# Kernel tuning notes

Hardware: AMD Instinct MI355X
Metric: run time of the kernel (lower is better)

## Reference

```python
import jax, jax.numpy as jnp
import numpy as np

EPS = 1e-7
N, L, BATCH = 512, 2, 128
N_IPF = 10


def setup_inputs() -> dict:
    key = jax.random.key(0)
    k1, k2, k3, k4 = jax.random.split(key, 4)
    return {
        "x": jax.random.randint(k1, (BATCH, N), 0, L, dtype=jnp.int32),
        "W": jax.random.normal(k2, (N, N), dtype=jnp.float32),
        "V_compress": jax.random.normal(k3, (N, L), dtype=jnp.float32),
        "E_compress": jax.random.normal(k4, (N, N, L, L), dtype=jnp.float32),
    }


def _moat_forward(W, V_compress, E_compress, x):
    n, l = V_compress.shape
    # marginals / joints
    V = jax.nn.softmax(V_compress, axis=1)              # (n, l)
    E = jnp.exp(E_compress)                              # (n, n, l, l)
    E = E / E.sum(axis=(-2, -1), keepdims=True)

    # 10-step Sinkhorn / IPF projection onto marginals V
    A_b = V[:, None, :, None]                            # (n, 1, l, 1)
    B_b = V[None, :, None, :]                            # (1, n, 1, l)
    for _ in range(N_IPF):
        row_marg = E.sum(axis=3, keepdims=True) + EPS    # (n, n, l, 1)
        col_marg = E.sum(axis=2, keepdims=True) + EPS    # (n, n, 1, l)
        E = E * (A_b / row_marg)
        E = E * (B_b / col_marg)
        E = E / (E.sum(axis=(-2, -1), keepdims=True) + EPS)

    # zero the diagonal (i == j) pairwise joints, clamp
    E = E * (1.0 - jnp.eye(n, dtype=E.dtype))[:, :, None, None]
    E = jnp.clip(E, 0.0, 1.0)

    # symmetric edge-weight matrix from strictly-lower-triangular sigmoid(W)
    Wm = jax.nn.sigmoid(W)
    Wm = jnp.tril(Wm, k=-1)
    Wm = Wm.T + Wm                                       # (n, n), zero diag
    L_0 = -Wm + jnp.diag(Wm.sum(axis=1))                 # graph Laplacian

    idx = jnp.arange(n)
    # Pr[b, i] = V[i, x[b, i]]
    Pr = V[idx[None, :], x]                              # (batch, n)
    # P[b, i, j] = E[i, j, x[b, i], x[b, j]]
    P = E[idx[None, :, None], idx[None, None, :], x[:, :, None], x[:, None, :]]  # (batch, n, n)
    P = P / (Pr[:, :, None] * Pr[:, None, :])

    WP = Wm[None, :, :] * P                              # (batch, n, n)
    Lb = -WP + jax.vmap(jnp.diag)(WP.sum(axis=2))        # batched Laplacian

    # matrix-tree theorem: logdet of the (n-1, n-1) principal minor
    _, logdet_L = jnp.linalg.slogdet(Lb[:, 1:, 1:])
    _, logdet_L0 = jnp.linalg.slogdet(L_0[1:, 1:])
    return jnp.log(Pr).sum(axis=1) + logdet_L - logdet_L0  # (batch,)


def reference(x, W, V_compress, E_compress):
    return _moat_forward(W, V_compress, E_compress, x)
```

## Files before the change

kernel.cpp:

```cpp
#include <hip/hip_runtime.h>
#include <hip/hip_bf16.h>
#include <math.h>

#define NDIM 512
#define NB   128
#define NMAT 129
#define EPSF 1e-7f
#define MS  ((size_t)262144)
#define LTS ((size_t)32768)
#define PSTR ((size_t)524288)

#define OFF_E   ((size_t)0)
#define OFF_WM  ((size_t)1048576)
#define OFF_IPR ((size_t)1310720)
#define OFF_LPR ((size_t)1376256)
#define OFF_LD  ((size_t)1376384)
#define OFF_MAT ((size_t)1377792)
#define OFF_LT  ((size_t)(OFF_MAT + (size_t)NMAT*MS))

__device__ __forceinline__ float rdlane(float v, int l) {
  return __uint_as_float((unsigned)__builtin_amdgcn_readlane((int)__float_as_uint(v), l));
}

__global__ __launch_bounds__(256) void k_prep(const float* __restrict__ W, const float* __restrict__ Vc,
                                              const float* __restrict__ Ec, float* __restrict__ Wm,
                                              float* __restrict__ E2) {
  int idx = blockIdx.x * 256 + threadIdx.x;
  int i = idx >> 9, j = idx & 511;
  float wv = 0.f;
  if (i > j)      wv = 1.f / (1.f + expf(-W[i*NDIM + j]));
  else if (i < j) wv = 1.f / (1.f + expf(-W[j*NDIM + i]));
  Wm[idx] = wv;
  float vi0 = Vc[2*i], vi1 = Vc[2*i+1];
  float mi = fmaxf(vi0, vi1);
  float ei0 = expf(vi0 - mi), ei1 = expf(vi1 - mi);
  float si = ei0 + ei1;
  float A0 = ei0 / si, A1 = ei1 / si;
  float vj0 = Vc[2*j], vj1 = Vc[2*j+1];
  float mj = fmaxf(vj0, vj1);
  float ej0 = expf(vj0 - mj), ej1 = expf(vj1 - mj);
  float sj = ej0 + ej1;
  float B0 = ej0 / sj, B1 = ej1 / sj;
  float4 ec = reinterpret_cast<const float4*>(Ec)[idx];
  float e00 = expf(ec.x), e01 = expf(ec.y), e10 = expf(ec.z), e11 = expf(ec.w);
  float s = e00 + e01 + e10 + e11;
  float inv = 1.f / s;
  e00 *= inv; e01 *= inv; e10 *= inv; e11 *= inv;
  for (int t = 0; t < 10; ++t) {
    float rm0 = e00 + e01 + EPSF, rm1 = e10 + e11 + EPSF;
    float cm0 = e00 + e10 + EPSF, cm1 = e01 + e11 + EPSF;
    float f0 = A0 / rm0, f1 = A1 / rm1;
    e00 *= f0; e01 *= f0; e10 *= f1; e11 *= f1;
    float g0 = B0 / cm0, g1 = B1 / cm1;
    e00 *= g0; e10 *= g0; e01 *= g1; e11 *= g1;
    float ss = e00 + e01 + e10 + e11 + EPSF;
    float iv = 1.f / ss;
    e00 *= iv; e01 *= iv; e10 *= iv; e11 *= iv;
  }
  if (i == j) { e00 = 0.f; e01 = 0.f; e10 = 0.f; e11 = 0.f; }
  e00 = fminf(fmaxf(e00, 0.f), 1.f);
  e01 = fminf(fmaxf(e01, 0.f), 1.f);
  e10 = fminf(fmaxf(e10, 0.f), 1.f);
  e11 = fminf(fmaxf(e11, 0.f), 1.f);
  reinterpret_cast<float2*>(E2)[idx]        = make_float2(e00, e01);
  reinterpret_cast<float2*>(E2 + PSTR)[idx] = make_float2(e10, e11);
}

__global__ __launch_bounds__(256) void k_Pr(const int* __restrict__ x, const float* __restrict__ Vc,
                                            float* __restrict__ invPr, float* __restrict__ logPr) {
  const int b = blockIdx.x;
  const int tid = threadIdx.x;
  float acc = 0.f;
  for (int ii = tid; ii < NDIM; ii += 256) {
    const int xv = x[b*NDIM + ii];
    float v0 = Vc[2*ii], v1 = Vc[2*ii+1];
    float mx = fmaxf(v0, v1);
    float e0 = expf(v0 - mx), e1 = expf(v1 - mx);
    float s = e0 + e1;
    const float p = xv ? (e1 / s) : (e0 / s);
    invPr[b*NDIM + ii] = 1.f / p;
    acc += logf(p);
  }
  for (int off = 32; off > 0; off >>= 1) acc += __shfl_down(acc, off, 64);
  __shared__ float sw[4];
  if ((tid & 63) == 0) sw[tid >> 6] = acc;
  __syncthreads();
  if (tid == 0) logPr[b] = sw[0] + sw[1] + sw[2] + sw[3];
}

__global__ __launch_bounds__(512) void k_build(const int* __restrict__ x, const float* __restrict__ E2,
                                               const float* __restrict__ Wm, const float* __restrict__ invPr,
                                               float* __restrict__ Mall) {
  const int b = blockIdx.x;
  const int i = blockIdx.y*8 + (threadIdx.x >> 6);
  const int lane = threadIdx.x & 63;
  const int j0 = lane << 3;

  const float4 w0 = *(const float4*)(Wm + (size_t)i*NDIM + j0);
  const float4 w1 = *(const float4*)(Wm + (size_t)i*NDIM + j0 + 4);
  float wp[8];
  if (b < NB) {
    const int   xi   = x[b*NDIM + i];
    const float ipri = invPr[b*NDIM + i];
    const int4  xa = *(const int4*)(x + b*NDIM + j0);
    const int4  xb = *(const int4*)(x + b*NDIM + j0 + 4);
    const float4 pa = *(const float4*)(invPr + b*NDIM + j0);
    const float4 pb = *(const float4*)(invPr + b*NDIM + j0 + 4);
    const float* pl = E2 + (size_t)xi*PSTR + ((size_t)i*NDIM + j0)*2;
    const float4 ea = *(const float4*)(pl);
    const float4 eb = *(const float4*)(pl + 4);
    const float4 ec = *(const float4*)(pl + 8);
    const float4 ed = *(const float4*)(pl + 12);
    wp[0] = w0.x * (xa.x ? ea.y : ea.x) * pa.x;
    wp[1] = w0.y * (xa.y ? ea.w : ea.z) * pa.y;
    wp[2] = w0.z * (xa.z ? eb.y : eb.x) * pa.z;
    wp[3] = w0.w * (xa.w ? eb.w : eb.z) * pa.w;
    wp[4] = w1.x * (xb.x ? ec.y : ec.x) * pb.x;
    wp[5] = w1.y * (xb.y ? ec.w : ec.z) * pb.y;
    wp[6] = w1.z * (xb.z ? ed.y : ed.x) * pb.z;
    wp[7] = w1.w * (xb.w ? ed.w : ed.z) * pb.w;
    #pragma unroll
    for (int k = 0; k < 8; ++k) wp[k] *= ipri;
  } else {
    wp[0]=w0.x; wp[1]=w0.y; wp[2]=w0.z; wp[3]=w0.w;
    wp[4]=w1.x; wp[5]=w1.y; wp[6]=w1.z; wp[7]=w1.w;
  }
  float s = ((wp[0]+wp[1])+(wp[2]+wp[3])) + ((wp[4]+wp[5])+(wp[6]+wp[7]));
  #pragma unroll
  for (int off = 32; off > 0; off >>= 1) s += __shfl_xor(s, off, 64);

  float o[8];
  #pragma unroll
  for (int k = 0; k < 8; ++k) o[k] = -wp[k];
  if (i == 0) {
    #pragma unroll
    for (int k = 0; k < 8; ++k) o[k] = 0.f;
    if (lane == 0) o[0] = 1.f;
  } else {
    if (lane == 0) o[0] = 0.f;
    #pragma unroll
    for (int k = 0; k < 8; ++k)
      if (j0 + k == i) o[k] = s;
  }
  float* dst = Mall + (size_t)b*MS + (size_t)i*NDIM + j0;
  *(float4*)(dst)   = make_float4(o[0],o[1],o[2],o[3]);
  *(float4*)(dst+4) = make_float4(o[4],o[5],o[6],o[7]);
}

template<int KK>
struct WFact {
  static __device__ __forceinline__ void run(float (&a)[64], const int lane,
                                             float& mypiv, float& myrec) {
    const float piv = rdlane(a[KK], KK);
    const float rec = 1.0f / piv;
    if (lane == KK) { mypiv = piv; myrec = rec; }
    if (lane > KK) {
      const float l = a[KK] * rec;
      a[KK] = l;
      #pragma unroll
      for (int c = KK + 1; c < 64; ++c)
        a[c] -= l * rdlane(a[c], KK);
    }
    WFact<KK + 1>::run(a, lane, mypiv, myrec);
  }
};
template<>
struct WFact<64> {
  static __device__ __forceinline__ void run(float (&)[64], int, float&, float&) {}
};

template<int C>
struct SolveStep {
  static __device__ __forceinline__ void run(float (&a)[64], const float (*T)[68]) {
    const float* Trow = T[C];
    float acc = a[C];
    #pragma unroll
    for (int p4 = 0; p4 + 4 <= C; p4 += 4) {
      const float4 tv = *(const float4*)(Trow + p4);
      acc -= a[p4+0] * tv.x;
      acc -= a[p4+1] * tv.y;
      acc -= a[p4+2] * tv.z;
      acc -= a[p4+3] * tv.w;
    }
    #pragma unroll
    for (int p = C & ~3; p < C; ++p) acc -= a[p] * Trow[p];
    a[C] = acc * Trow[66];
    SolveStep<C + 1>::run(a, T);
  }
};
template<>
struct SolveStep<64> {
  static __device__ __forceinline__ void run(float (&)[64], const float (*)[68]) {}
};

__global__ __launch_bounds__(128) void k_panel(float* __restrict__ Mall, float* __restrict__ Lt,
                                               float* __restrict__ logdets, int k0, int mrem) {
  const int b = blockIdx.x;
  const int sub = blockIdx.y;
  float* __restrict__ M = Mall + (size_t)b*MS;
  float* __restrict__ L = Lt + (size_t)b*LTS;
  const int t = threadIdx.x;
  __shared__ __align__(16) float T[64][68];

  if (t < 64) {
    float a[64];
    const float* row = M + (size_t)(k0+t)*NDIM + k0;
    #pragma unroll
    for (int c4 = 0; c4 < 16; ++c4) {
      float4 v = *(const float4*)(row + c4*4);
      a[c4*4+0]=v.x; a[c4*4+1]=v.y; a[c4*4+2]=v.z; a[c4*4+3]=v.w;
    }
    float mypiv = 1.f, myrec = 1.f;
    WFact<0>::run(a, t, mypiv, myrec);
    #pragma unroll
    for (int c = 0; c < 64; ++c) T[c][t] = a[c];
    T[t][66] = myrec;
    if (sub == 0) {
      float v = logf(fabsf(mypiv));
      #pragma unroll
      for (int off = 32; off > 0; off >>= 1) v += __shfl_down(v, off, 64);
      if (t == 0) logdets[b] = (k0 == 0) ? v : (logdets[b] + v);
    }
  }
  __syncthreads();

  if (mrem > 0) {
    if (t < 64) {
      const int col = k0 + 64 + sub*64 + t;
      float u[64];
      #pragma unroll
      for (int r = 0; r < 64; ++r) u[r] = M[(size_t)(k0+r)*NDIM + col];
      #pragma unroll
      for (int p = 0; p < 63; ++p) {
        const float lv = u[p];
        const float* Trow = T[p];
        const int kk0 = p + 1;
        const int kkA = (p + 4) & ~3;
        #pragma unroll
        for (int kk = kk0; kk < kkA; ++kk) u[kk] -= Trow[kk] * lv;
        #pragma unroll
        for (int kk4 = kkA; kk4 < 64; kk4 += 4) {
          const float4 tv = *(const float4*)(Trow + kk4);
          u[kk4+0] -= tv.x * lv;
          u[kk4+1] -= tv.y * lv;
          u[kk4+2] -= tv.z * lv;
          u[kk4+3] -= tv.w * lv;
        }
      }
      #pragma unroll
      for (int r = 1; r < 64; ++r) M[(size_t)(k0+r)*NDIM + col] = u[r];
    } else {
      const int lr = 64 + sub*64 + (t - 64);
      const int gr = k0 + lr;
      float a[64];
      const float* row = M + (size_t)gr*NDIM + k0;
      #pragma unroll
      for (int c4 = 0; c4 < 16; ++c4) {
        float4 v = *(const float4*)(row + c4*4);
        a[c4*4+0]=v.x; a[c4*4+1]=v.y; a[c4*4+2]=v.z; a[c4*4+3]=v.w;
      }
      SolveStep<0>::run(a, T);
      #pragma unroll
      for (int c = 0; c < 64; ++c) L[(size_t)c*NDIM + lr] = a[c];
    }
  }
}

__global__ __launch_bounds__(256, 4) void k_gemm(float* __restrict__ Mall, const float* __restrict__ Lt,
                                                 int k0) {
  const int b = blockIdx.x;
  float* __restrict__ M = Mall + (size_t)b*MS;
  const float* __restrict__ L = Lt + (size_t)b*LTS;
  __shared__ __align__(16) float As[64][68];
  __shared__ __align__(16) float Bs[64][68];
  const int tid = threadIdx.x;
  const int tx = tid & 15, ty = tid >> 4;
  const int rowbase = 64 + blockIdx.y*64;
  const int colbase = 64 + blockIdx.z*64;
  #pragma unroll
  for (int i = 0; i < 4; ++i) {
    int q = tid + 256*i;
    int p = q >> 4, f = q & 15;
    *(float4*)&As[p][f*4] = *(const float4*)&L[(size_t)p*NDIM + rowbase + f*4];
    *(float4*)&Bs[p][f*4] = *(const float4*)&M[(size_t)(k0+p)*NDIM + (k0+colbase) + f*4];
  }
  float* Crow = M + (size_t)(k0+rowbase+ty*4)*NDIM + (k0+colbase+tx*4);
  float4 c0 = *(float4*)(Crow + 0*NDIM);
  float4 c1 = *(float4*)(Crow + 1*NDIM);
  float4 c2 = *(float4*)(Crow + 2*NDIM);
  float4 c3 = *(float4*)(Crow + 3*NDIM);
  __syncthreads();
  #pragma unroll
  for (int p = 0; p < 64; ++p) {
    const float4 av = *(const float4*)&As[p][ty*4];
    const float4 bv = *(const float4*)&Bs[p][tx*4];
    c0.x -= av.x*bv.x; c0.y -= av.x*bv.y; c0.z -= av.x*bv.z; c0.w -= av.x*bv.w;
    c1.x -= av.y*bv.x; c1.y -= av.y*bv.y; c1.z -= av.y*bv.z; c1.w -= av.y*bv.w;
    c2.x -= av.z*bv.x; c2.y -= av.z*bv.y; c2.z -= av.z*bv.z; c2.w -= av.z*bv.w;
    c3.x -= av.w*bv.x; c3.y -= av.w*bv.y; c3.z -= av.w*bv.z; c3.w -= av.w*bv.w;
  }
  *(float4*)(Crow + 0*NDIM) = c0;
  *(float4*)(Crow + 1*NDIM) = c1;
  *(float4*)(Crow + 2*NDIM) = c2;
  *(float4*)(Crow + 3*NDIM) = c3;
}

__global__ void k_final(const float* __restrict__ logPr, const float* __restrict__ logdets,
                        float* __restrict__ out) {
  int t = threadIdx.x;
  if (t < NB) out[t] = logPr[t] + logdets[t] - logdets[NB];
}

extern "C" void kernel_launch(void* const* d_in, const int* in_sizes, int n_in,
                              void* d_out, int out_size, void* d_ws, size_t ws_size,
                              hipStream_t stream) {
  const int*   x  = (const int*)  d_in[0];
  const float* W  = (const float*)d_in[1];
  const float* Vc = (const float*)d_in[2];
  const float* Ec = (const float*)d_in[3];
  float* out = (float*)d_out;
  float* ws  = (float*)d_ws;
  (void)in_sizes; (void)n_in; (void)out_size; (void)ws_size;

  float* Mat = ws + OFF_MAT;
  float* Lt  = ws + OFF_LT;
  float* Ld  = ws + OFF_LD;

  k_prep<<<1024, 256, 0, stream>>>(W, Vc, Ec, ws + OFF_WM, ws + OFF_E);
  k_Pr  <<<NB,   256, 0, stream>>>(x, Vc, ws + OFF_IPR, ws + OFF_LPR);
  dim3 gb(NMAT, 64);
  k_build<<<gb, 512, 0, stream>>>(x, ws + OFF_E, ws + OFF_WM, ws + OFF_IPR, Mat);

  for (int s = 0; s < 8; ++s) {
    const int k0 = s*64;
    const int mrem = NDIM - k0 - 64;
    dim3 gp(NMAT, (mrem > 0) ? (mrem/64) : 1);
    k_panel<<<gp, 128, 0, stream>>>(Mat, Lt, Ld, k0, mrem);
    if (mrem > 0) {
      const int nt = mrem/64;
      dim3 gg(NMAT, nt, nt);
      k_gemm<<<gg, 256, 0, stream>>>(Mat, Lt, k0);
    }
  }
  k_final<<<1, 128, 0, stream>>>(ws + OFF_LPR, Ld, out);
}
```

Baseline: 570.2 us.

## Fuse last three LU panel/GEMM steps into one shared-memory tail kernel

```diff
diff --git a/kernel.cpp b/kernel.cpp
--- a/kernel.cpp
+++ b/kernel.cpp
@@ -305,6 +305,125 @@
   *(float4*)(Crow + 3*NDIM) = c3;
 }
 
+#define SLD 196
+__global__ __launch_bounds__(512) void k_tail(float* __restrict__ Mall, float* __restrict__ logdets,
+                                              int k0) {
+  extern __shared__ float Sp[];
+  const int b = blockIdx.x;
+  float* __restrict__ M = Mall + (size_t)b*MS;
+  const int t = threadIdx.x;
+
+  for (int idx = t; idx < 192*48; idx += 512) {
+    const int r = idx / 48, q = idx - r*48;
+    *(float4*)&Sp[r*SLD + q*4] = *(const float4*)&M[(size_t)(k0+r)*NDIM + k0 + q*4];
+  }
+  float base = 0.f;
+  if (t == 0) base = logdets[b];
+  __syncthreads();
+
+  for (int step = 0; step < 3; ++step) {
+    const int d0 = step*64;
+    const int nrem = 128 - d0;
+
+    if (t < 64) {
+      float a[64];
+      const float* row = Sp + (d0+t)*SLD + d0;
+      #pragma unroll
+      for (int c4 = 0; c4 < 16; ++c4) {
+        float4 v = *(const float4*)(row + c4*4);
+        a[c4*4+0]=v.x; a[c4*4+1]=v.y; a[c4*4+2]=v.z; a[c4*4+3]=v.w;
+      }
+      float mypiv = 1.f, myrec = 1.f;
+      WFact<0>::run(a, t, mypiv, myrec);
+      #pragma unroll
+      for (int c = 0; c < 64; ++c) Sp[(size_t)(d0+c)*SLD + d0 + t] = a[c];
+      Sp[(size_t)(d0+t)*SLD + d0 + t] = myrec;
+      float v = logf(fabsf(mypiv));
+      #pragma unroll
+      for (int off = 32; off > 0; off >>= 1) v += __shfl_down(v, off, 64);
+      if (t == 0) base += v;
+    }
+    __syncthreads();
+
+    if (nrem > 0) {
+      if (t < nrem) {
+        const int col = d0 + 64 + t;
+        float u[64];
+        #pragma unroll
+        for (int r = 0; r < 64; ++r) u[r] = Sp[(d0+r)*SLD + col];
+        #pragma unroll
+        for (int p = 0; p < 63; ++p) {
+          const float lv = u[p];
+          const float* Trow = Sp + (d0+p)*SLD + d0;
+          #pragma unroll
+          for (int kk = p+1; kk < 64; ++kk) u[kk] -= Trow[kk] * lv;
+        }
+        #pragma unroll
+        for (int r = 1; r < 64; ++r) Sp[(d0+r)*SLD + col] = u[r];
+      } else if (t >= 256 && t < 256 + nrem) {
+        const int gr = d0 + 64 + (t - 256);
+        float* row = Sp + gr*SLD + d0;
+        float a[64];
+        #pragma unroll
+        for (int c4 = 0; c4 < 16; ++c4) {
+          float4 v = *(const float4*)(row + c4*4);
+          a[c4*4+0]=v.x; a[c4*4+1]=v.y; a[c4*4+2]=v.z; a[c4*4+3]=v.w;
+        }
+        for (int C = 0; C < 64; ++C) {
+          const float* Trow = Sp + (d0+C)*SLD + d0;
+          float acc = a[C];
+          for (int p = 0; p < C; ++p) acc -= a[p] * Trow[p];
+          a[C] = acc * Trow[C];
+        }
+        #pragma unroll
+        for (int c4 = 0; c4 < 16; ++c4)
+          *(float4*)(row + c4*4) = make_float4(a[c4*4],a[c4*4+1],a[c4*4+2],a[c4*4+3]);
+      }
+      __syncthreads();
+
+      if (nrem == 128) {
+        const int tx = t & 31, ty = t >> 5;
+        const int rbase = d0 + 64 + ty*8;
+        const int cb = d0 + 64 + tx*4;
+        float4 cr[8];
+        #pragma unroll
+        for (int k = 0; k < 8; ++k) cr[k] = *(float4*)&Sp[(rbase+k)*SLD + cb];
+        #pragma unroll
+        for (int p = 0; p < 64; ++p) {
+          const float4 uv = *(const float4*)&Sp[(d0+p)*SLD + cb];
+          #pragma unroll
+          for (int k = 0; k < 8; ++k) {
+            const float lv = Sp[(rbase+k)*SLD + d0 + p];
+            cr[k].x -= lv*uv.x; cr[k].y -= lv*uv.y; cr[k].z -= lv*uv.z; cr[k].w -= lv*uv.w;
+          }
+        }
+        #pragma unroll
+        for (int k = 0; k < 8; ++k) *(float4*)&Sp[(rbase+k)*SLD + cb] = cr[k];
+      } else {
+        const int tx = t & 15, ty = t >> 4;
+        const int rbase = d0 + 64 + ty*2;
+        const int cb = d0 + 64 + tx*4;
+        float4 cr[2];
+        #pragma unroll
+        for (int k = 0; k < 2; ++k) cr[k] = *(float4*)&Sp[(rbase+k)*SLD + cb];
+        #pragma unroll
+        for (int p = 0; p < 64; ++p) {
+          const float4 uv = *(const float4*)&Sp[(d0+p)*SLD + cb];
+          #pragma unroll
+          for (int k = 0; k < 2; ++k) {
+            const float lv = Sp[(rbase+k)*SLD + d0 + p];
+            cr[k].x -= lv*uv.x; cr[k].y -= lv*uv.y; cr[k].z -= lv*uv.z; cr[k].w -= lv*uv.w;
+          }
+        }
+        #pragma unroll
+        for (int k = 0; k < 2; ++k) *(float4*)&Sp[(rbase+k)*SLD + cb] = cr[k];
+      }
+      __syncthreads();
+    }
+  }
+  if (t == 0) logdets[b] = base;
+}
+
 __global__ void k_final(const float* __restrict__ logPr, const float* __restrict__ logdets,
                         float* __restrict__ out) {
   int t = threadIdx.x;
@@ -326,21 +445,28 @@
   float* Lt  = ws + OFF_LT;
   float* Ld  = ws + OFF_LD;
 
+  static bool attr_set = false;
+  if (!attr_set) {
+    (void)hipFuncSetAttribute((const void*)k_tail,
+                              hipFuncAttributeMaxDynamicSharedMemorySize, 192*SLD*4);
+    attr_set = true;
+  }
+
   k_prep<<<1024, 256, 0, stream>>>(W, Vc, Ec, ws + OFF_WM, ws + OFF_E);
   k_Pr  <<<NB,   256, 0, stream>>>(x, Vc, ws + OFF_IPR, ws + OFF_LPR);
   dim3 gb(NMAT, 64);
   k_build<<<gb, 512, 0, stream>>>(x, ws + OFF_E, ws + OFF_WM, ws + OFF_IPR, Mat);
 
-  for (int s = 0; s < 8; ++s) {
+  for (int s = 0; s < 5; ++s) {
     const int k0 = s*64;
     const int mrem = NDIM - k0 - 64;
-    dim3 gp(NMAT, (mrem > 0) ? (mrem/64) : 1);
+    dim3 gp(NMAT, mrem/64);
     k_panel<<<gp, 128, 0, stream>>>(Mat, Lt, Ld, k0, mrem);
-    if (mrem > 0) {
-      const int nt = mrem/64;
-      dim3 gg(NMAT, nt, nt);
-      k_gemm<<<gg, 256, 0, stream>>>(Mat, Lt, k0);
-    }
-  }
+    const int nt = mrem/64;
+    dim3 gg(NMAT, nt, nt);
+    k_gemm<<<gg, 256, 0, stream>>>(Mat, Lt, k0);
+  }
+  k_tail<<<NMAT, 512, 192*SLD*4, stream>>>(Mat, Ld, 320);
+
   k_final<<<1, 128, 0, stream>>>(ws + OFF_LPR, Ld, out);
 }
```

New measurement: 1.183 ms. 2.07x slower.
